# Kernel tuning notes

Measured on AMD Instinct MI355X. Metric: run time of the kernel, lower is better.

## Reference

```python
import jax, jax.numpy as jnp
import numpy as np


def setup_inputs() -> dict:
    key = jax.random.key(0)
    ks = jax.random.split(key, 7)
    B, S, E, N, H = 2, 2048, 1024, 8, 4096
    scale = 0.02
    return {
        "x": jax.random.normal(ks[0], (B, S, E), dtype=jnp.float32),
        "Wr": jax.random.normal(ks[1], (E, N), dtype=jnp.float32) * scale,
        "br": jnp.zeros((N,), dtype=jnp.float32),
        "W1": jax.random.normal(ks[2], (N, E, H), dtype=jnp.float32) * scale,
        "b1": jnp.zeros((N, H), dtype=jnp.float32),
        "W2": jax.random.normal(ks[3], (N, H, E), dtype=jnp.float32) * scale,
        "b2": jnp.zeros((N, E), dtype=jnp.float32),
        "top_k": 2,
    }


def reference(x, Wr, br, W1, b1, W2, b2, top_k):
    # Router: logits [B,S,N], keep top-k, softmax over the kept entries.
    logits = jnp.einsum("bse,en->bsn", x, Wr) + br
    _, idx = jax.lax.top_k(logits, top_k)                      # [B,S,k]
    mask = jax.nn.one_hot(idx, logits.shape[-1], dtype=jnp.bool_).any(-2)  # [B,S,N]
    masked = jnp.where(mask, logits, -jnp.inf)
    weights = jax.nn.softmax(masked, axis=-1)                   # [B,S,N]

    # Dense all-experts FFN (faithful to original): every expert on every token.
    # hid: [B,S,N,H]
    hid = jax.nn.gelu(jnp.einsum("bse,neh->bsnh", x, W1) + b1, approximate=False)
    expert_out = jnp.einsum("bsnh,nhe->bsne", hid, W2) + b2    # [B,S,N,E]
    # dropout is identity in eval mode

    # Weighted combine over experts.
    return jnp.einsum("bsne,bsn->bse", expert_out, weights)
```

## Files before the change

kernel.cpp:

```cpp
#include <hip/hip_runtime.h>
#include <hip/hip_bf16.h>
#include <cmath>
#include <cstdint>


typedef unsigned short u16;
typedef __attribute__((ext_vector_type(8))) short bf16x8;
typedef __attribute__((ext_vector_type(4))) float f32x4;
typedef __attribute__((ext_vector_type(8))) unsigned short us8;
typedef __attribute__((ext_vector_type(4))) unsigned short us4;

#define TOKENS  4096
#define EDIM    1024
#define NEXP    8
#define HDIM    4096
#define MAXROWS 8192
#define ROWPAD  384
#define MAXTILES 40
#define RBLK    1024

#define MFMA16(va, vb, vc) __builtin_amdgcn_mfma_f32_16x16x32_bf16(va, vb, vc, 0, 0, 0)

__device__ __forceinline__ u16 f2bf(float f) {
  __hip_bfloat16 h = __float2bfloat16(f);
  return *reinterpret_cast<u16*>(&h);
}
__device__ __forceinline__ int clampk(int k) {
  return k < 1 ? 1 : (k > 8 ? 8 : k);
}
__device__ __forceinline__ void async16(void* lds, const void* g) {
  __builtin_amdgcn_global_load_lds((const __attribute__((address_space(1))) void*)g,
                                   (__attribute__((address_space(3))) void*)lds,
                                   16, 0, 0);
}
__device__ __forceinline__ float gelu_f(float v) {
  const float z = fabsf(v) * 0.70710678118654752f;
  const float t = __builtin_amdgcn_rcpf(fmaf(0.3275911f, z, 1.0f));
  const float p = t * fmaf(t, fmaf(t, fmaf(t, fmaf(t, 1.061405429f, -1.453152027f),
                                           1.421413741f), -0.284496736f), 0.254829592f);
  float er = 1.0f - p * __expf(-z * z);
  er = copysignf(er, v);
  return 0.5f * v * (1.0f + er);
}
__device__ __forceinline__ int xcd_swz(int orig, int nwg) {
  const int q = nwg >> 3, r = nwg & 7;
  const int x = orig & 7, l = orig >> 3;
  return (x < r ? x * (q + 1) : r * (q + 1) + (x - r) * q) + l;
}

__global__ void router_k(const float* __restrict__ x, const float* __restrict__ Wr,
                         const float* __restrict__ br, const int* __restrict__ topk_p,
                         int* __restrict__ sel_e, float* __restrict__ sel_w,
                         int* __restrict__ sel_lpos, int* __restrict__ hist_blk) {
  __shared__ int wsel[4][8];
  const int blk = blockIdx.x;
  const int tid = threadIdx.x;
  const int wv = tid >> 6, ln = tid & 63;
  const int t = blk * 4 + wv;
  const int k = clampk(topk_p[0]);
  float acc[NEXP];
#pragma unroll
  for (int n = 0; n < NEXP; ++n) acc[n] = 0.f;
  const float* xr = x + (size_t)t * EDIM;
  for (int ei = ln; ei < EDIM; ei += 64) {
    float xv = xr[ei];
    float4 w0 = *(const float4*)(Wr + ei * NEXP);
    float4 w1 = *(const float4*)(Wr + ei * NEXP + 4);
    acc[0] += xv * w0.x; acc[1] += xv * w0.y; acc[2] += xv * w0.z; acc[3] += xv * w0.w;
    acc[4] += xv * w1.x; acc[5] += xv * w1.y; acc[6] += xv * w1.z; acc[7] += xv * w1.w;
  }
#pragma unroll
  for (int s = 32; s > 0; s >>= 1) {
#pragma unroll
    for (int n = 0; n < NEXP; ++n) acc[n] += __shfl_down(acc[n], s);
  }
  if (ln == 0) {
    float logit[NEXP];
#pragma unroll
    for (int n = 0; n < NEXP; ++n) logit[n] = acc[n] + br[n];
    bool used[NEXP];
#pragma unroll
    for (int n = 0; n < NEXP; ++n) used[n] = false;
    int se[NEXP]; float sw[NEXP];
    for (int j = 0; j < k; ++j) {
      int bi = 0; float bv = -INFINITY;
      for (int n = 0; n < NEXP; ++n)
        if (!used[n] && logit[n] > bv) { bv = logit[n]; bi = n; }
      used[bi] = true; se[j] = bi; sw[j] = bv;
    }
    float mx = sw[0], sum = 0.f;
    for (int j = 0; j < k; ++j) { sw[j] = expf(sw[j] - mx); sum += sw[j]; }
    float inv = 1.f / sum;
    for (int j = 0; j < k; ++j) {
      sel_e[t * 8 + j] = se[j];
      sel_w[t * 8 + j] = sw[j] * inv;
      wsel[wv][j] = se[j];
    }
  }
  __syncthreads();
  if (tid == 0) {
    int h[NEXP];
#pragma unroll
    for (int e = 0; e < NEXP; ++e) h[e] = 0;
    for (int w = 0; w < 4; ++w)
      for (int j = 0; j < k; ++j) {
        int e = wsel[w][j];
        sel_lpos[(blk * 4 + w) * 8 + j] = h[e]++;
      }
#pragma unroll
    for (int e = 0; e < NEXP; ++e) hist_blk[blk * NEXP + e] = h[e];
  }
}

__global__ void scan_k(const int* __restrict__ hist_blk, int* __restrict__ counts,
                       int* __restrict__ offsets, int* __restrict__ blk_base,
                       int* __restrict__ tmap) {
  __shared__ int sc[NEXP][257];
  __shared__ int offs[NEXP];
  const int tid = threadIdx.x;
  int h[4][NEXP], part[NEXP];
#pragma unroll
  for (int e = 0; e < NEXP; ++e) part[e] = 0;
#pragma unroll
  for (int r = 0; r < 4; ++r) {
    const int row = tid * 4 + r;
#pragma unroll
    for (int e = 0; e < NEXP; ++e) { h[r][e] = hist_blk[row * NEXP + e]; part[e] += h[r][e]; }
  }
#pragma unroll
  for (int e = 0; e < NEXP; ++e) sc[e][tid] = part[e];
  __syncthreads();
  for (int d = 1; d < 256; d <<= 1) {
    int v[NEXP];
#pragma unroll
    for (int e = 0; e < NEXP; ++e) v[e] = (tid >= d) ? sc[e][tid - d] : 0;
    __syncthreads();
#pragma unroll
    for (int e = 0; e < NEXP; ++e) sc[e][tid] += v[e];
    __syncthreads();
  }
  if (tid == 0) {
    int s = 0;
    for (int e = 0; e < NEXP; ++e) {
      int tot = sc[e][255];
      offsets[e] = s; offs[e] = s; counts[e] = tot; s += tot;
    }
    int nt = 0;
    for (int e = 0; e < NEXP; ++e) {
      int nb = (counts[e] + 255) >> 8;
      for (int b = 0; b < nb && nt < MAXTILES; ++b) tmap[nt++] = (e << 16) | b;
    }
    for (; nt < MAXTILES; ++nt) tmap[nt] = -1;
  }
  __syncthreads();
#pragma unroll
  for (int e = 0; e < NEXP; ++e) {
    int run = offs[e] + sc[e][tid] - part[e];
#pragma unroll
    for (int r = 0; r < 4; ++r) {
      blk_base[(tid * 4 + r) * NEXP + e] = run;
      run += h[r][e];
    }
  }
}

__global__ void finalize_k(const int* __restrict__ sel_e, const int* __restrict__ sel_lpos,
                           const int* __restrict__ blk_base, const int* __restrict__ topk_p,
                           int* __restrict__ sel_pos, int* __restrict__ row_token) {
  const int k = clampk(topk_p[0]);
  const int i = blockIdx.x * 256 + threadIdx.x;
  if (i >= TOKENS * k) return;
  const int t = i / k, j = i - t * k;
  const int e = sel_e[t * 8 + j];
  const int pos = blk_base[(t >> 2) * NEXP + e] + sel_lpos[t * 8 + j];
  sel_pos[t * 8 + j] = pos;
  row_token[pos] = t;
}

__global__ void gather_cast_k(const float* __restrict__ x, const int* __restrict__ row_token,
                              const int* __restrict__ counts, u16* __restrict__ xg) {
  __shared__ int tot_s;
  if (threadIdx.x == 0) {
    int t = 0;
#pragma unroll
    for (int e = 0; e < NEXP; ++e) t += counts[e];
    tot_s = t;
  }
  __syncthreads();
  const int row = blockIdx.x;
  u16* dst = xg + (size_t)row * EDIM;
  const int i = threadIdx.x;
  if (row >= tot_s) {
    us4 z = {0, 0, 0, 0};
    *(us4*)(dst + i * 4) = z;
    return;
  }
  const float* src = x + (size_t)row_token[row] * EDIM;
  float4 v = *(const float4*)(src + i * 4);
  us4 o; o[0] = f2bf(v.x); o[1] = f2bf(v.y); o[2] = f2bf(v.z); o[3] = f2bf(v.w);
  *(us4*)(dst + i * 4) = o;
}

__global__ void zero_f32_k(float* __restrict__ p) {
  const size_t i = ((size_t)blockIdx.x * 256 + threadIdx.x) * 4;
  float4 z = {0.f, 0.f, 0.f, 0.f};
  *(float4*)(p + i) = z;
}

__global__ void transpose_k(const float* __restrict__ W1, const float* __restrict__ W2,
                            u16* __restrict__ W1t, u16* __restrict__ W2t,
                            int full, int h0c) {
  __shared__ __align__(16) u16 T[64][68];
  const int z = blockIdx.z;
  int mat, e, h0;
  if (full) { mat = z < 32 ? 0 : 1; int zz = mat ? z - 32 : z; e = zz >> 2; h0 = (zz & 3) * 1024; }
  else      { mat = z < 8 ? 0 : 1;  e = mat ? z - 8 : z;      h0 = h0c; }
  const size_t oes = full ? (size_t)HDIM * EDIM : (size_t)1024 * 1024;
  const float* in; size_t istride;
  if (mat == 0) { in = W1 + (size_t)e * EDIM * HDIM + h0;            istride = HDIM; }
  else          { in = W2 + (size_t)e * HDIM * EDIM + (size_t)h0 * EDIM; istride = EDIM; }
  const int r0 = blockIdx.y * 64, c0 = blockIdx.x * 64;
  const int tid = threadIdx.x;
#pragma unroll
  for (int it = 0; it < 4; ++it) {
    int cell = it * 256 + tid;
    int rl = cell >> 4, c4 = (cell & 15) * 4;
    float4 v = *(const float4*)(in + (size_t)(r0 + rl) * istride + c0 + c4);
    us4 o; o[0] = f2bf(v.x); o[1] = f2bf(v.y); o[2] = f2bf(v.z); o[3] = f2bf(v.w);
    *(us4*)&T[rl][c4] = o;
  }
  __syncthreads();
#pragma unroll
  for (int it = 0; it < 2; ++it) {
    int cell = it * 256 + tid;
    int cl = cell >> 3, r8 = (cell & 7) * 8;
    us8 o;
#pragma unroll
    for (int j = 0; j < 8; ++j) o[j] = T[r8 + j][cl];
    u16* out;
    if (mat == 0) {
      int orow = (full ? h0 : 0) + c0 + cl;
      out = W1t + (size_t)e * oes + (size_t)orow * 1024 + r0 + r8;
    } else {
      int ost = full ? HDIM : 1024;
      out = W2t + (size_t)e * oes + (size_t)(c0 + cl) * ost + (full ? h0 : 0) + r0 + r8;
    }
    *(us8*)out = o;
  }
}

template <int MODE>
__global__ __launch_bounds__(512, 2) void gemm256_k(
    const u16* __restrict__ A, int astride, int kblocks,
    const u16* __restrict__ Bt, size_t b_estride, int bstride,
    const float* __restrict__ bias, int bias_dim, int bias_col0, int bias_on,
    const int* __restrict__ counts, const int* __restrict__ offsets,
    const int* __restrict__ tmap, int NB,
    u16* __restrict__ hid, int hid_stride, float* __restrict__ Y) {
  __shared__ __align__(16) char lds_s[131072];
  const int bid = xcd_swz(blockIdx.x, gridDim.x);
  const int by  = blockIdx.y;
  const int tile = bid / NB;
  const int tv = tmap[tile];
  if (tv < 0) return;
  const int n0 = (bid - tile * NB) << 8;
  const int e = tv >> 16;
  const int m0 = (tv & 0xffff) << 8;
  const int cnt = counts[e], off_e = offsets[e];

  const int tid = threadIdx.x;
  const int wv = tid >> 6, ln = tid & 63;
  const int wm = wv >> 2, wn = wv & 3;

  const int trow = tid >> 3;
  const int swz  = (tid & 7) ^ (trow & 7);
  const size_t koff = (size_t)by * kblocks * 64;
  const u16* gA = A + (size_t)(off_e + m0 + trow) * astride + koff + swz * 8;
  const u16* gB = Bt + (size_t)e * b_estride + (size_t)(n0 + trow) * bstride + koff + swz * 8;
  const size_t a64 = (size_t)astride * 64;
  const size_t b64 = (size_t)bstride * 64;
  char* const lA = lds_s + wv * 1024;
  char* const lB = lds_s + 65536 + wv * 1024;

  auto stA = [&](int buf, int h, int kt) {
    const u16* g = gA + (size_t)(2 * h) * a64 + (size_t)kt * 64;
    char* l = lA + (buf << 15) + (h << 14);
    async16(l, g);
    async16(l + 8192, g + a64);
  };
  auto stB = [&](int buf, int h, int kt) {
    const u16* g = gB + (size_t)(2 * h) * b64 + (size_t)kt * 64;
    char* l = lB + (buf << 15) + (h << 14);
    async16(l, g);
    async16(l + 8192, g + b64);
  };

  const int r15 = ln & 15, quad = ln >> 4, rs = r15 & 7;
  const int a_k0 = (wm * 128 + r15) * 128 + (((quad    ) ^ rs) << 4);
  const int a_k1 = (wm * 128 + r15) * 128 + (((quad + 4) ^ rs) << 4);
  const int b_k0 = (wn *  64 + r15) * 128 + (((quad    ) ^ rs) << 4);
  const int b_k1 = (wn *  64 + r15) * 128 + (((quad + 4) ^ rs) << 4);

  f32x4 acc[8][4];
#pragma unroll
  for (int i = 0; i < 8; ++i)
#pragma unroll
    for (int j = 0; j < 4; ++j) acc[i][j] = (f32x4){0.f, 0.f, 0.f, 0.f};

  bf16x8 a0[4], a1[4], b0[4], b1[4];

  stB(0, 0, 0); stB(0, 1, 0);
  stA(0, 0, 0); stA(0, 1, 0);
  if (kblocks > 1) {
    stB(1, 0, 1); stB(1, 1, 1);
    asm volatile("s_waitcnt vmcnt(4)" ::: "memory");
  } else {
    asm volatile("s_waitcnt vmcnt(0)" ::: "memory");
  }
  __builtin_amdgcn_s_barrier();

  for (int t = 0; t < kblocks; ++t) {
    const int cb = (t & 1) << 15;
    const int nx = (t & 1) ^ 1;
    const char* cA = lds_s + cb;
    const char* cB = lds_s + 65536 + cb;

#pragma unroll
    for (int mi = 0; mi < 4; ++mi) {
      a0[mi] = *(const bf16x8*)(cA + a_k0 + mi * 2048);
      a1[mi] = *(const bf16x8*)(cA + a_k1 + mi * 2048);
    }
#pragma unroll
    for (int ni = 0; ni < 2; ++ni) {
      b0[ni] = *(const bf16x8*)(cB + b_k0 + ni * 2048);
      b1[ni] = *(const bf16x8*)(cB + b_k1 + ni * 2048);
    }
    if (t + 1 < kblocks) stA(nx, 0, t + 1);
    asm volatile("s_waitcnt lgkmcnt(8)" ::: "memory");
    __builtin_amdgcn_s_barrier();
    asm volatile("s_waitcnt lgkmcnt(0)" ::: "memory");
    __builtin_amdgcn_s_setprio(1);
#pragma unroll
    for (int mi = 0; mi < 4; ++mi)
#pragma unroll
      for (int ni = 0; ni < 2; ++ni) {
        acc[mi][ni] = MFMA16(a0[mi], b0[ni], acc[mi][ni]);
        acc[mi][ni] = MFMA16(a1[mi], b1[ni], acc[mi][ni]);
      }
    __builtin_amdgcn_s_setprio(0);
    __builtin_amdgcn_s_barrier();

#pragma unroll
    for (int ni = 2; ni < 4; ++ni) {
      b0[ni] = *(const bf16x8*)(cB + b_k0 + ni * 2048);
      b1[ni] = *(const bf16x8*)(cB + b_k1 + ni * 2048);
    }
    if (t + 1 < kblocks) stA(nx, 1, t + 1);
    __builtin_amdgcn_s_barrier();
    asm volatile("s_waitcnt lgkmcnt(0)" ::: "memory");
    __builtin_amdgcn_s_setprio(1);
#pragma unroll
    for (int mi = 0; mi < 4; ++mi)
#pragma unroll
      for (int ni = 2; ni < 4; ++ni) {
        acc[mi][ni] = MFMA16(a0[mi], b0[ni], acc[mi][ni]);
        acc[mi][ni] = MFMA16(a1[mi], b1[ni], acc[mi][ni]);
      }
    __builtin_amdgcn_s_setprio(0);
    __builtin_amdgcn_s_barrier();

#pragma unroll
    for (int mi = 0; mi < 4; ++mi) {
      a0[mi] = *(const bf16x8*)(cA + a_k0 + (mi + 4) * 2048);
      a1[mi] = *(const bf16x8*)(cA + a_k1 + (mi + 4) * 2048);
    }
    if (t + 2 < kblocks) stB(t & 1, 0, t + 2);
    __builtin_amdgcn_s_barrier();
    asm volatile("s_waitcnt lgkmcnt(0)" ::: "memory");
    __builtin_amdgcn_s_setprio(1);
#pragma unroll
    for (int mi = 0; mi < 4; ++mi)
#pragma unroll
      for (int ni = 0; ni < 2; ++ni) {
        acc[mi + 4][ni] = MFMA16(a0[mi], b0[ni], acc[mi + 4][ni]);
        acc[mi + 4][ni] = MFMA16(a1[mi], b1[ni], acc[mi + 4][ni]);
      }
    __builtin_amdgcn_s_setprio(0);
    __builtin_amdgcn_s_barrier();

    if (t + 2 < kblocks) {
      stB(t & 1, 1, t + 2);
      asm volatile("s_waitcnt vmcnt(4)" ::: "memory");
    } else {
      asm volatile("s_waitcnt vmcnt(0)" ::: "memory");
    }
    __builtin_amdgcn_s_barrier();
    __builtin_amdgcn_s_setprio(1);
#pragma unroll
    for (int mi = 0; mi < 4; ++mi)
#pragma unroll
      for (int ni = 2; ni < 4; ++ni) {
        acc[mi + 4][ni] = MFMA16(a0[mi], b0[ni], acc[mi + 4][ni]);
        acc[mi + 4][ni] = MFMA16(a1[mi], b1[ni], acc[mi + 4][ni]);
      }
    __builtin_amdgcn_s_setprio(0);
    __builtin_amdgcn_s_barrier();
  }

  const int col0 = n0 + wn * 64 + r15;
  float bv[4];
#pragma unroll
  for (int ni = 0; ni < 4; ++ni) {
    const float b = bias[(size_t)e * bias_dim + bias_col0 + col0 + ni * 16];
    bv[ni] = (MODE == 0) ? b : ((bias_on && by == 0) ? b : 0.f);
  }
#pragma unroll
  for (int mi = 0; mi < 8; ++mi) {
    const int mb = m0 + wm * 128 + mi * 16 + quad * 4;
#pragma unroll
    for (int ni = 0; ni < 4; ++ni) {
      const int nc = col0 + ni * 16;
#pragma unroll
      for (int r = 0; r < 4; ++r) {
        const int m = mb + r;
        if (m < cnt) {
          const float v = acc[mi][ni][r] + bv[ni];
          if (MODE == 0) {
            hid[(size_t)(off_e + m) * hid_stride + nc] = f2bf(gelu_f(v));
          } else {
            atomicAdd(&Y[(size_t)(off_e + m) * EDIM + nc], v);
          }
        }
      }
    }
  }
}

__global__ void combine_k(const float* __restrict__ Y, const int* __restrict__ sel_pos,
                          const float* __restrict__ sel_w, const int* __restrict__ topk_p,
                          float* __restrict__ out) {
  const int t = blockIdx.x;
  const int tid = threadIdx.x;
  const int k = clampk(topk_p[0]);
  float a0 = 0.f, a1 = 0.f, a2 = 0.f, a3 = 0.f;
  for (int j = 0; j < k; ++j) {
    const float w = sel_w[t * 8 + j];
    const size_t row = (size_t)sel_pos[t * 8 + j];
    const float4 v = *(const float4*)(Y + row * EDIM + tid * 4);
    a0 += w * v.x; a1 += w * v.y; a2 += w * v.z; a3 += w * v.w;
  }
  float4 o; o.x = a0; o.y = a1; o.z = a2; o.w = a3;
  *(float4*)(out + (size_t)t * EDIM + tid * 4) = o;
}

extern "C" void kernel_launch(void* const* d_in, const int* in_sizes, int n_in,
                              void* d_out, int out_size, void* d_ws, size_t ws_size,
                              hipStream_t stream) {
  const float* x   = (const float*)d_in[0];
  const float* Wr  = (const float*)d_in[1];
  const float* br  = (const float*)d_in[2];
  const float* W1  = (const float*)d_in[3];
  const float* b1  = (const float*)d_in[4];
  const float* W2  = (const float*)d_in[5];
  const float* b2  = (const float*)d_in[6];
  const int* topk  = (const int*)d_in[7];
  float* out = (float*)d_out;

  char* ws = (char*)d_ws;
  size_t o = 0;
  auto alloc = [&](size_t bytes) -> char* {
    char* p = ws + o; o += (bytes + 255) & ~(size_t)255; return p;
  };
  int*   counts    = (int*)alloc(NEXP * 4);
  int*   offsets   = (int*)alloc(NEXP * 4);
  int*   tmap      = (int*)alloc(MAXTILES * 4);
  int*   sel_e     = (int*)alloc((size_t)TOKENS * 8 * 4);
  int*   sel_pos   = (int*)alloc((size_t)TOKENS * 8 * 4);
  int*   sel_lpos  = (int*)alloc((size_t)TOKENS * 8 * 4);
  float* sel_w     = (float*)alloc((size_t)TOKENS * 8 * 4);
  int*   row_token = (int*)alloc((size_t)TOKENS * 8 * 4);
  int*   hist_blk  = (int*)alloc((size_t)RBLK * NEXP * 4);
  int*   blk_base  = (int*)alloc((size_t)RBLK * NEXP * 4);
  u16*   xg        = (u16*)alloc((size_t)(MAXROWS + ROWPAD) * EDIM * 2);
  float* Y         = (float*)alloc((size_t)MAXROWS * EDIM * 4);

  const size_t full_need  = ((size_t)NEXP * HDIM * EDIM * 2) * 2
                          + (size_t)(MAXROWS + ROWPAD) * HDIM * 2 + 4096;
  const bool full = (ws_size - o) >= full_need;
  u16 *W1t, *W2t, *hid;
  if (full) {
    W1t = (u16*)alloc((size_t)NEXP * HDIM * EDIM * 2);
    W2t = (u16*)alloc((size_t)NEXP * HDIM * EDIM * 2);
    hid = (u16*)alloc((size_t)(MAXROWS + ROWPAD) * HDIM * 2);
  } else {
    W1t = (u16*)alloc((size_t)NEXP * 1024 * 1024 * 2);
    W2t = (u16*)alloc((size_t)NEXP * 1024 * 1024 * 2);
    hid = (u16*)alloc((size_t)(MAXROWS + ROWPAD) * 1024 * 2);
  }

  zero_f32_k<<<dim3((MAXROWS * EDIM) / 1024), dim3(256), 0, stream>>>(Y);
  router_k<<<dim3(RBLK), dim3(256), 0, stream>>>(x, Wr, br, topk,
                                                 sel_e, sel_w, sel_lpos, hist_blk);
  scan_k<<<dim3(1), dim3(256), 0, stream>>>(hist_blk, counts, offsets, blk_base, tmap);
  finalize_k<<<dim3(TOKENS * 8 / 256), dim3(256), 0, stream>>>(sel_e, sel_lpos, blk_base,
                                                               topk, sel_pos, row_token);
  gather_cast_k<<<dim3(MAXROWS + ROWPAD), dim3(256), 0, stream>>>(x, row_token, counts, xg);

  if (full) {
    transpose_k<<<dim3(16, 16, 64), dim3(256), 0, stream>>>(W1, W2, W1t, W2t, 1, 0);
    gemm256_k<0><<<dim3(MAXTILES * 16, 1), dim3(512), 0, stream>>>(
        xg, EDIM, 16, W1t, (size_t)HDIM * EDIM, EDIM,
        b1, HDIM, 0, 1, counts, offsets, tmap, 16, hid, HDIM, nullptr);
    gemm256_k<1><<<dim3(MAXTILES * 4, 4), dim3(512), 0, stream>>>(
        hid, HDIM, 16, W2t, (size_t)HDIM * EDIM, HDIM,
        b2, EDIM, 0, 1, counts, offsets, tmap, 4, nullptr, 0, Y);
  } else {
    for (int c = 0; c < 4; ++c) {
      const int h0 = c * 1024;
      transpose_k<<<dim3(16, 16, 16), dim3(256), 0, stream>>>(W1, W2, W1t, W2t, 0, h0);
      gemm256_k<0><<<dim3(MAXTILES * 4, 1), dim3(512), 0, stream>>>(
          xg, EDIM, 16, W1t, (size_t)1024 * 1024, 1024,
          b1, HDIM, h0, 1, counts, offsets, tmap, 4, hid, 1024, nullptr);
      gemm256_k<1><<<dim3(MAXTILES * 4, 1), dim3(512), 0, stream>>>(
          hid, 1024, 16, W2t, (size_t)1024 * 1024, 1024,
          b2, EDIM, 0, (c == 0) ? 1 : 0, counts, offsets, tmap, 4, nullptr, 0, Y);
    }
  }
  combine_k<<<dim3(TOKENS), dim3(256), 0, stream>>>(Y, sel_pos, sel_w, topk, out);
}
```

Measured before the change: 687.6 us.

## Simplify GEMM pipeline to single-stage double buffering and fuse Y zeroing into gather

Replaces the hand-tuned, finely interleaved GEMM main loop with a simple double-buffered loop. Each k-step now issues one prefetch of the next A and B tiles and runs all MFMAs between plain __syncthreads barriers, dropping the split half-tile staging, explicit vmcnt/lgkmcnt waits, and setprio hints. It also removes the XCD-aware block swizzle and folds the zeroing of Y into gather_cast_k, which saves one kernel launch. The simpler schedule gives up overlap between LDS reads, global loads and MFMA issue, and losing the swizzle may hurt L2 locality across XCDs.

After: 661.5 us. -3.8%, faster.

```diff
diff --git a/kernel.cpp b/kernel.cpp
--- a/kernel.cpp
+++ b/kernel.cpp
@@ -41,11 +41,6 @@
   float er = 1.0f - p * __expf(-z * z);
   er = copysignf(er, v);
   return 0.5f * v * (1.0f + er);
-}
-__device__ __forceinline__ int xcd_swz(int orig, int nwg) {
-  const int q = nwg >> 3, r = nwg & 7;
-  const int x = orig & 7, l = orig >> 3;
-  return (x < r ? x * (q + 1) : r * (q + 1) + (x - r) * q) + l;
 }
 
 __global__ void router_k(const float* __restrict__ x, const float* __restrict__ Wr,
@@ -178,7 +173,8 @@
 }
 
 __global__ void gather_cast_k(const float* __restrict__ x, const int* __restrict__ row_token,
-                              const int* __restrict__ counts, u16* __restrict__ xg) {
+                              const int* __restrict__ counts, u16* __restrict__ xg,
+                              float* __restrict__ Y) {
   __shared__ int tot_s;
   if (threadIdx.x == 0) {
     int t = 0;
@@ -186,10 +182,14 @@
     for (int e = 0; e < NEXP; ++e) t += counts[e];
     tot_s = t;
   }
-  __syncthreads();
   const int row = blockIdx.x;
+  const int i = threadIdx.x;
+  if (row < MAXROWS) {
+    float4 z = {0.f, 0.f, 0.f, 0.f};
+    *(float4*)(Y + (size_t)row * EDIM + i * 4) = z;
+  }
+  __syncthreads();
   u16* dst = xg + (size_t)row * EDIM;
-  const int i = threadIdx.x;
   if (row >= tot_s) {
     us4 z = {0, 0, 0, 0};
     *(us4*)(dst + i * 4) = z;
@@ -199,12 +199,6 @@
   float4 v = *(const float4*)(src + i * 4);
   us4 o; o[0] = f2bf(v.x); o[1] = f2bf(v.y); o[2] = f2bf(v.z); o[3] = f2bf(v.w);
   *(us4*)(dst + i * 4) = o;
-}
-
-__global__ void zero_f32_k(float* __restrict__ p) {
-  const size_t i = ((size_t)blockIdx.x * 256 + threadIdx.x) * 4;
-  float4 z = {0.f, 0.f, 0.f, 0.f};
-  *(float4*)(p + i) = z;
 }
 
 __global__ void transpose_k(const float* __restrict__ W1, const float* __restrict__ W2,
@@ -258,7 +252,7 @@
     const int* __restrict__ tmap, int NB,
     u16* __restrict__ hid, int hid_stride, float* __restrict__ Y) {
   __shared__ __align__(16) char lds_s[131072];
-  const int bid = xcd_swz(blockIdx.x, gridDim.x);
+  const int bid = blockIdx.x;
   const int by  = blockIdx.y;
   const int tile = bid / NB;
   const int tv = tmap[tile];
@@ -282,17 +276,15 @@
   char* const lA = lds_s + wv * 1024;
   char* const lB = lds_s + 65536 + wv * 1024;
 
-  auto stA = [&](int buf, int h, int kt) {
-    const u16* g = gA + (size_t)(2 * h) * a64 + (size_t)kt * 64;
-    char* l = lA + (buf << 15) + (h << 14);
-    async16(l, g);
-    async16(l + 8192, g + a64);
-  };
-  auto stB = [&](int buf, int h, int kt) {
-    const u16* g = gB + (size_t)(2 * h) * b64 + (size_t)kt * 64;
-    char* l = lB + (buf << 15) + (h << 14);
-    async16(l, g);
-    async16(l + 8192, g + b64);
+  auto stage = [&](int buf, int kt) {
+    const u16* ga = gA + (size_t)kt * 64;
+    const u16* gb = gB + (size_t)kt * 64;
+    char* la = lA + (buf << 15);
+    char* lb = lB + (buf << 15);
+#pragma unroll
+    for (int h = 0; h < 4; ++h) async16(la + h * 8192, ga + (size_t)h * a64);
+#pragma unroll
+    for (int h = 0; h < 4; ++h) async16(lb + h * 8192, gb + (size_t)h * b64);
   };
 
   const int r15 = ln & 15, quad = ln >> 4, rs = r15 & 7;
@@ -309,19 +301,11 @@
 
   bf16x8 a0[4], a1[4], b0[4], b1[4];
 
-  stB(0, 0, 0); stB(0, 1, 0);
-  stA(0, 0, 0); stA(0, 1, 0);
-  if (kblocks > 1) {
-    stB(1, 0, 1); stB(1, 1, 1);
-    asm volatile("s_waitcnt vmcnt(4)" ::: "memory");
-  } else {
-    asm volatile("s_waitcnt vmcnt(0)" ::: "memory");
-  }
-  __builtin_amdgcn_s_barrier();
+  stage(0, 0);
+  __syncthreads();
 
   for (int t = 0; t < kblocks; ++t) {
     const int cb = (t & 1) << 15;
-    const int nx = (t & 1) ^ 1;
     const char* cA = lds_s + cb;
     const char* cB = lds_s + 65536 + cb;
 
@@ -331,80 +315,33 @@
       a1[mi] = *(const bf16x8*)(cA + a_k1 + mi * 2048);
     }
 #pragma unroll
-    for (int ni = 0; ni < 2; ++ni) {
+    for (int ni = 0; ni < 4; ++ni) {
       b0[ni] = *(const bf16x8*)(cB + b_k0 + ni * 2048);
       b1[ni] = *(const bf16x8*)(cB + b_k1 + ni * 2048);
     }
-    if (t + 1 < kblocks) stA(nx, 0, t + 1);
-    asm volatile("s_waitcnt lgkmcnt(8)" ::: "memory");
-    __builtin_amdgcn_s_barrier();
-    asm volatile("s_waitcnt lgkmcnt(0)" ::: "memory");
-    __builtin_amdgcn_s_setprio(1);
+    if (t + 1 < kblocks) stage((t & 1) ^ 1, t + 1);
+
 #pragma unroll
     for (int mi = 0; mi < 4; ++mi)
 #pragma unroll
-      for (int ni = 0; ni < 2; ++ni) {
+      for (int ni = 0; ni < 4; ++ni) {
         acc[mi][ni] = MFMA16(a0[mi], b0[ni], acc[mi][ni]);
         acc[mi][ni] = MFMA16(a1[mi], b1[ni], acc[mi][ni]);
       }
-    __builtin_amdgcn_s_setprio(0);
-    __builtin_amdgcn_s_barrier();
-
-#pragma unroll
-    for (int ni = 2; ni < 4; ++ni) {
-      b0[ni] = *(const bf16x8*)(cB + b_k0 + ni * 2048);
-      b1[ni] = *(const bf16x8*)(cB + b_k1 + ni * 2048);
-    }
-    if (t + 1 < kblocks) stA(nx, 1, t + 1);
-    __builtin_amdgcn_s_barrier();
-    asm volatile("s_waitcnt lgkmcnt(0)" ::: "memory");
-    __builtin_amdgcn_s_setprio(1);
-#pragma unroll
-    for (int mi = 0; mi < 4; ++mi)
-#pragma unroll
-      for (int ni = 2; ni < 4; ++ni) {
-        acc[mi][ni] = MFMA16(a0[mi], b0[ni], acc[mi][ni]);
-        acc[mi][ni] = MFMA16(a1[mi], b1[ni], acc[mi][ni]);
-      }
-    __builtin_amdgcn_s_setprio(0);
-    __builtin_amdgcn_s_barrier();
 
 #pragma unroll
     for (int mi = 0; mi < 4; ++mi) {
       a0[mi] = *(const bf16x8*)(cA + a_k0 + (mi + 4) * 2048);
       a1[mi] = *(const bf16x8*)(cA + a_k1 + (mi + 4) * 2048);
     }
-    if (t + 2 < kblocks) stB(t & 1, 0, t + 2);
-    __builtin_amdgcn_s_barrier();
-    asm volatile("s_waitcnt lgkmcnt(0)" ::: "memory");
-    __builtin_amdgcn_s_setprio(1);
 #pragma unroll
     for (int mi = 0; mi < 4; ++mi)
 #pragma unroll
-      for (int ni = 0; ni < 2; ++ni) {
+      for (int ni = 0; ni < 4; ++ni) {
         acc[mi + 4][ni] = MFMA16(a0[mi], b0[ni], acc[mi + 4][ni]);
         acc[mi + 4][ni] = MFMA16(a1[mi], b1[ni], acc[mi + 4][ni]);
       }
-    __builtin_amdgcn_s_setprio(0);
-    __builtin_amdgcn_s_barrier();
-
-    if (t + 2 < kblocks) {
-      stB(t & 1, 1, t + 2);
-      asm volatile("s_waitcnt vmcnt(4)" ::: "memory");
-    } else {
-      asm volatile("s_waitcnt vmcnt(0)" ::: "memory");
-    }
-    __builtin_amdgcn_s_barrier();
-    __builtin_amdgcn_s_setprio(1);
-#pragma unroll
-    for (int mi = 0; mi < 4; ++mi)
-#pragma unroll
-      for (int ni = 2; ni < 4; ++ni) {
-        acc[mi + 4][ni] = MFMA16(a0[mi], b0[ni], acc[mi + 4][ni]);
-        acc[mi + 4][ni] = MFMA16(a1[mi], b1[ni], acc[mi + 4][ni]);
-      }
-    __builtin_amdgcn_s_setprio(0);
-    __builtin_amdgcn_s_barrier();
+    __syncthreads();
   }
 
   const int col0 = n0 + wn * 64 + r15;
@@ -498,13 +435,13 @@
     hid = (u16*)alloc((size_t)(MAXROWS + ROWPAD) * 1024 * 2);
   }
 
-  zero_f32_k<<<dim3((MAXROWS * EDIM) / 1024), dim3(256), 0, stream>>>(Y);
   router_k<<<dim3(RBLK), dim3(256), 0, stream>>>(x, Wr, br, topk,
                                                  sel_e, sel_w, sel_lpos, hist_blk);
   scan_k<<<dim3(1), dim3(256), 0, stream>>>(hist_blk, counts, offsets, blk_base, tmap);
   finalize_k<<<dim3(TOKENS * 8 / 256), dim3(256), 0, stream>>>(sel_e, sel_lpos, blk_base,
                                                                topk, sel_pos, row_token);
-  gather_cast_k<<<dim3(MAXROWS + ROWPAD), dim3(256), 0, stream>>>(x, row_token, counts, xg);
+  gather_cast_k<<<dim3(MAXROWS + ROWPAD), dim3(256), 0, stream>>>(x, row_token, counts,
+                                                                  xg, Y);
 
   if (full) {
     transpose_k<<<dim3(16, 16, 64), dim3(256), 0, stream>>>(W1, W2, W1t, W2t, 1, 0);
```
